# Optimization experiments

Hardware: AMD Instinct MI355X
Metric: run time of the kernel (lower is better)

Reference implementation:

```python
import jax, jax.numpy as jnp
import numpy as np

EPS = 1e-5      # F.layer_norm default eps
ALPHA = 0.08    # ALALLaDA blend coefficient


def setup_inputs() -> dict:
    key = jax.random.key(0)
    ks = jax.random.split(key, 6)
    B, S, D, K = 2, 2048, 2048, 8
    Fh = D // 4
    h_L = jax.random.normal(ks[0], (B, S, D), jnp.float32)
    # nonzero -> masked position (stands in for input_ids == 126336)
    mask = jax.random.randint(ks[1], (B, S), 0, 2).astype(jnp.int32)
    Wr = jax.random.normal(ks[2], (K, D), jnp.float32) / np.sqrt(D).astype(np.float32)
    br = jnp.zeros((K,), jnp.float32)
    W1 = jax.random.normal(ks[3], (K, D, Fh), jnp.float32) / np.sqrt(D).astype(np.float32)
    b1 = jnp.zeros((K, Fh), jnp.float32)
    W2 = jax.random.normal(ks[4], (K, Fh, D), jnp.float32) / np.sqrt(Fh).astype(np.float32)
    b2 = jnp.zeros((K, D), jnp.float32)
    return {"h_L": h_L, "mask": mask, "Wr": Wr, "br": br,
            "W1": W1, "b1": b1, "W2": W2, "b2": b2, "range_r": 8}


def _router_blend(h_L, Wr, br, W1, b1, W2, b2, mask, range_r):
    B, S, D = h_L.shape
    masked = mask != 0
    um = (~masked).astype(h_L.dtype)  # unmasked validity [B,S]
    # Per-token, per-expert outputs M[b,s,k,d]: Linear -> exact GELU -> Linear.
    pre = jnp.einsum('bsd,kdf->bskf', h_L, W1) + b1
    M = jnp.einsum('bskf,kfd->bskd', jax.nn.gelu(pre, approximate=False), W2) + b2
    # Routing weights at every position (softmax over K experts).
    w = jax.nn.softmax(jnp.einsum('bsd,kd->bsk', h_L, Wr) + br, axis=-1)
    # Accumulate weighted expert outputs over the +/-range_r neighbor window,
    # counting only unmasked neighbors. Fixed small loop over 2r offsets.
    num = jnp.zeros((B, S, D), h_L.dtype)
    cnt = jnp.zeros((B, S), h_L.dtype)
    for o in range(-range_r, range_r + 1):
        if o == 0:
            continue
        if o > 0:  # neighbor t = a + o: shift left, zero-pad tail
            Mo = jnp.pad(M[:, o:], ((0, 0), (0, o), (0, 0), (0, 0)))
            vo = jnp.pad(um[:, o:], ((0, 0), (0, o)))
        else:      # neighbor t = a + o (o<0): shift right, zero-pad head
            Mo = jnp.pad(M[:, :o], ((0, 0), (-o, 0), (0, 0), (0, 0)))
            vo = jnp.pad(um[:, :o], ((0, 0), (-o, 0)))
        num = num + vo[..., None] * jnp.einsum('bsk,bskd->bsd', w, Mo)
        cnt = cnt + vo
    has = cnt > 0
    mean = num / jnp.maximum(cnt, 1.0)[..., None]   # mean over valid neighbors
    # layer_norm over d_model, no affine
    mu = mean.mean(-1, keepdims=True)
    var = jnp.mean((mean - mu) ** 2, axis=-1, keepdims=True)
    ln = (mean - mu) / jnp.sqrt(var + EPS)
    # delta is written only at masked positions that had >=1 neighbor
    delta = jnp.where((masked & has)[..., None], ln, 0.0)
    return h_L + ALPHA * delta


def reference(h_L, mask, Wr, br, W1, b1, W2, b2, range_r):
    return _router_blend(h_L, Wr, br, W1, b1, W2, b2, mask, range_r)
```

## Files before the change

kernel.cpp:

```cpp
#include <hip/hip_runtime.h>
#include <hip/hip_bf16.h>
#include <math.h>


#define ALPHA 0.08f
#define EPS 1e-5f

typedef __attribute__((ext_vector_type(8))) __bf16 bf16x8;
typedef __attribute__((ext_vector_type(8))) short short8;
typedef __attribute__((ext_vector_type(4))) float f32x4;

__device__ __forceinline__ unsigned short f2bf(float f) {
  unsigned u = __float_as_uint(f);
  u += 0x7fffu + ((u >> 16) & 1u);
  return (unsigned short)(u >> 16);
}
__device__ __forceinline__ float bf2f(unsigned short b) {
  return __uint_as_float(((unsigned)b) << 16);
}

#define GLD16(gptr, lptr)                                                     \
  __builtin_amdgcn_global_load_lds(                                           \
      (const __attribute__((address_space(1))) void*)(gptr),                  \
      (__attribute__((address_space(3))) void*)(lptr), 16, 0, 0)

__device__ __forceinline__ int wave_incl_scan(int v, int lane) {
#pragma unroll
  for (int off = 1; off < 64; off <<= 1) {
    int t = __shfl_up(v, off);
    if (lane >= off) v += t;
  }
  return v;
}

__global__ __launch_bounds__(1024) void scan_kernel(
    const int* __restrict__ mask, const int* __restrict__ rptr,
    int* __restrict__ ru, int* __restrict__ unm_idx,
    int* __restrict__ msk_idx, int* __restrict__ pos2row,
    int* __restrict__ counts) {
  __shared__ int sru[4097];
  __shared__ int wsum[16];
  __shared__ int wsum2[17];
  const int tid = threadIdx.x;
  const int lane = tid & 63, wv = tid >> 6;
  const int t0 = tid * 4;
  const int4 m4 = *(const int4*)(mask + t0);
  int f[4];
  f[0] = (m4.x == 0); f[1] = (m4.y == 0); f[2] = (m4.z == 0); f[3] = (m4.w == 0);
  const int tsum = f[0] + f[1] + f[2] + f[3];
  const int isc = wave_incl_scan(tsum, lane);
  if (lane == 63) wsum[wv] = isc;
  __syncthreads();
  if (tid == 0) {
    int acc = 0;
#pragma unroll
    for (int i = 0; i < 16; ++i) { int v = wsum[i]; wsum[i] = acc; acc += v; }
    sru[4096] = acc;
    counts[0] = acc;
    ru[4096] = acc;
  }
  __syncthreads();
  int ex = wsum[wv] + isc - tsum;
#pragma unroll
  for (int j = 0; j < 4; ++j) {
    sru[t0 + j] = ex;
    ru[t0 + j] = ex;
    if (f[j]) unm_idx[ex] = t0 + j;
    ex += f[j];
  }
  __syncthreads();
  const int r = rptr[0];
  int mval[4] = {m4.x, m4.y, m4.z, m4.w};
  int g[4];
#pragma unroll
  for (int j = 0; j < 4; ++j) {
    const int t = t0 + j;
    const int s = t & 2047, tb = t & ~2047;
    const int lo = max(s - r, 0), hi = min(s + r, 2047);
    const int cnt = sru[tb + hi + 1] - sru[tb + lo];
    g[j] = (mval[j] != 0 && cnt > 0) ? 1 : 0;
  }
  const int tsum2 = g[0] + g[1] + g[2] + g[3];
  const int isc2 = wave_incl_scan(tsum2, lane);
  if (lane == 63) wsum2[wv] = isc2;
  __syncthreads();
  if (tid == 0) {
    int acc = 0;
#pragma unroll
    for (int i = 0; i < 16; ++i) { int v = wsum2[i]; wsum2[i] = acc; acc += v; }
    counts[1] = acc;
  }
  __syncthreads();
  int ex2 = wsum2[wv] + isc2 - tsum2;
#pragma unroll
  for (int j = 0; j < 4; ++j) {
    const int t = t0 + j;
    pos2row[t] = g[j] ? ex2 : -1;
    if (g[j]) msk_idx[ex2] = t;
    ex2 += g[j];
  }
}

__global__ void packrouter_kernel(const float* __restrict__ h,
                                  const int* __restrict__ mask,
                                  const int* __restrict__ ru,
                                  const float* __restrict__ Wr,
                                  const float* __restrict__ br,
                                  float* __restrict__ w,
                                  unsigned short* __restrict__ hbc) {
  const int a = blockIdx.x;
  const int tid = threadIdx.x;
  const int lane = tid & 63, wid = tid >> 6;
  const size_t base = (size_t)a * 2048;
  const int d0 = tid * 8;
  float hv[8];
  *(float4*)(hv) = *(const float4*)(h + base + d0);
  *(float4*)(hv + 4) = *(const float4*)(h + base + d0 + 4);
  float acc[8];
#pragma unroll
  for (int k = 0; k < 8; ++k) {
    float wvv[8];
    *(float4*)(wvv) = *(const float4*)(Wr + (size_t)k * 2048 + d0);
    *(float4*)(wvv + 4) = *(const float4*)(Wr + (size_t)k * 2048 + d0 + 4);
    float s = 0.f;
#pragma unroll
    for (int j = 0; j < 8; ++j) s += hv[j] * wvv[j];
    acc[k] = s;
  }
#pragma unroll
  for (int off = 32; off > 0; off >>= 1)
#pragma unroll
    for (int k = 0; k < 8; ++k) acc[k] += __shfl_down(acc[k], off);
  __shared__ float red[4][8];
  __shared__ float logits[8];
  if (lane == 0)
#pragma unroll
    for (int k = 0; k < 8; ++k) red[wid][k] = acc[k];
  __syncthreads();
  if (tid < 8)
    logits[tid] = red[0][tid] + red[1][tid] + red[2][tid] + red[3][tid] + br[tid];
  __syncthreads();
  if (tid == 0) {
    float mx = logits[0];
#pragma unroll
    for (int k = 1; k < 8; ++k) mx = fmaxf(mx, logits[k]);
    float e[8], se = 0.f;
#pragma unroll
    for (int k = 0; k < 8; ++k) {
      e[k] = expf(logits[k] - mx);
      se += e[k];
    }
    const float is = 1.f / se;
#pragma unroll
    for (int k = 0; k < 8; ++k) w[(size_t)a * 8 + k] = e[k] * is;
  }
  if (mask[a] == 0) {
    const int i = ru[a];
    short8 o;
#pragma unroll
    for (int j = 0; j < 8; ++j) o[j] = (short)f2bf(hv[j]);
    *(short8*)(hbc + (size_t)i * 2048 + d0) = o;
  }
}

__global__ void transpose_pack_kernel(const float* __restrict__ src,
                                      unsigned short* __restrict__ dst,
                                      int R, int C, size_t dstStride,
                                      size_t dstExpStride) {
  __shared__ float tile[32][33];
  const int k = blockIdx.z;
  src += (size_t)k * (size_t)R * (size_t)C;
  dst += (size_t)k * dstExpStride;
  const int c0 = blockIdx.x * 32;
  const int r0 = blockIdx.y * 32;
  const int tx = threadIdx.x;
  const int ty = threadIdx.y;
#pragma unroll
  for (int i = 0; i < 4; ++i)
    tile[ty + 8 * i][tx] = src[(size_t)(r0 + ty + 8 * i) * C + (c0 + tx)];
  __syncthreads();
#pragma unroll
  for (int i = 0; i < 4; ++i) {
    const int c = c0 + ty + 8 * i;
    dst[(size_t)c * dstStride + (size_t)(r0 + tx)] = f2bf(tile[tx][ty + 8 * i]);
  }
}

template <int EPI>
__global__ __launch_bounds__(256, 2) void gemm_bt_kernel(
    const unsigned short* __restrict__ A, const unsigned short* __restrict__ Bt,
    float* __restrict__ Cf, unsigned short* __restrict__ Cb,
    const float* __restrict__ bias, const int* __restrict__ counts, int cidx,
    int N, int Kd) {
  const int Mlim = counts[cidx];
  const int bm = blockIdx.y * 128;
  if (bm >= Mlim) return;
  __shared__ __align__(16) unsigned short L[4][8192];
  const int tid = threadIdx.x;
  const int lane = tid & 63;
  const int wid = tid >> 6;
  const int bn = blockIdx.x * 128;
  const int wr = wid >> 1;
  const int wc = wid & 1;

  f32x4 acc[4][4];
#pragma unroll
  for (int m = 0; m < 4; ++m)
#pragma unroll
    for (int n = 0; n < 4; ++n) acc[m][n] = (f32x4){0.f, 0.f, 0.f, 0.f};

  const int srow = wid * 16 + (lane >> 2);
  const int scol = (lane & 3) * 8;
  const unsigned short* gA0 = A + (size_t)(bm + srow) * Kd + scol;
  const unsigned short* gA1 = gA0 + (size_t)64 * Kd;
  const unsigned short* gB0 = Bt + (size_t)(bn + srow) * Kd + scol;
  const unsigned short* gB1 = gB0 + (size_t)64 * Kd;

  const int aoff = (wr * 64 + (lane & 15)) * 32 + (lane >> 4) * 8;
  const int boff = (wc * 64 + (lane & 15)) * 32 + (lane >> 4) * 8;

#define STAGE(buf, t)                                                         \
  {                                                                           \
    const int k0_ = (t) << 5;                                                 \
    unsigned short* la_ = &L[(buf)][0] + wid * 512;                           \
    unsigned short* lb_ = &L[(buf)][4096] + wid * 512;                        \
    GLD16(gA0 + k0_, la_);                                                    \
    GLD16(gA1 + k0_, la_ + 2048);                                             \
    GLD16(gB0 + k0_, lb_);                                                    \
    GLD16(gB1 + k0_, lb_ + 2048);                                             \
  }

#define COMPUTE(buf)                                                          \
  {                                                                           \
    const unsigned short* As_ = &L[(buf)][0];                                 \
    const unsigned short* Bs_ = &L[(buf)][4096];                              \
    bf16x8 af[4], bfr[4];                                                     \
    _Pragma("unroll") for (int m = 0; m < 4; ++m) af[m] =                     \
        __builtin_bit_cast(bf16x8, *(const short8*)(As_ + aoff + m * 512));   \
    _Pragma("unroll") for (int n = 0; n < 4; ++n) bfr[n] =                    \
        __builtin_bit_cast(bf16x8, *(const short8*)(Bs_ + boff + n * 512));   \
    _Pragma("unroll") for (int m = 0; m < 4; ++m)                             \
        _Pragma("unroll") for (int n = 0; n < 4; ++n) acc[m][n] =             \
            __builtin_amdgcn_mfma_f32_16x16x32_bf16(af[m], bfr[n],            \
                                                    acc[m][n], 0, 0, 0);      \
  }

  const int nt = Kd >> 5;
  STAGE(0, 0);
  STAGE(1, 1);
  STAGE(2, 2);
#pragma unroll 1
  for (int t = 0; t < nt - 3; ++t) {
    asm volatile("s_waitcnt vmcnt(8)" ::: "memory");
    __builtin_amdgcn_s_barrier();
    __builtin_amdgcn_sched_barrier(0);
    STAGE((t + 3) & 3, t + 3);
    COMPUTE(t & 3);
  }
  {
    asm volatile("s_waitcnt vmcnt(8)" ::: "memory");
    __builtin_amdgcn_s_barrier();
    __builtin_amdgcn_sched_barrier(0);
    COMPUTE((nt - 3) & 3);
  }
  {
    asm volatile("s_waitcnt vmcnt(4)" ::: "memory");
    __builtin_amdgcn_s_barrier();
    __builtin_amdgcn_sched_barrier(0);
    COMPUTE((nt - 2) & 3);
  }
  {
    asm volatile("s_waitcnt vmcnt(0)" ::: "memory");
    __builtin_amdgcn_s_barrier();
    __builtin_amdgcn_sched_barrier(0);
    COMPUTE((nt - 1) & 3);
  }
#undef STAGE
#undef COMPUTE

  const int r0 = bm + wr * 64 + (lane >> 4) * 4;
  const int c0 = bn + wc * 64 + (lane & 15);
#pragma unroll
  for (int m = 0; m < 4; ++m) {
#pragma unroll
    for (int n = 0; n < 4; ++n) {
      const int col = c0 + n * 16;
#pragma unroll
      for (int i = 0; i < 4; ++i) {
        const int row = r0 + m * 16 + i;
        if (row >= Mlim) continue;
        const size_t off = (size_t)row * N + col;
        float v = acc[m][n][i];
        if (EPI == 1) {
          v += bias[col];
          v = 0.5f * v * (1.0f + erff(v * 0.70710678118654752f));
          Cb[off] = f2bf(v);
        } else {
          Cf[off] = v;
        }
      }
    }
  }
}

__global__ void window_kernel(const unsigned short* __restrict__ Act_c,
                              const float* __restrict__ w,
                              const int* __restrict__ msk_idx,
                              const int* __restrict__ ru,
                              const int* __restrict__ rptr,
                              const int* __restrict__ counts,
                              unsigned short* __restrict__ G_c) {
  const int i = blockIdx.y;
  if (i >= counts[1]) return;
  const int a = msk_idx[i];
  const int s = a & 2047;
  const int tb = a & ~2047;
  const int r = rptr[0];
  const int lo = max(s - r, 0), hi = min(s + r, 2047);
  const int jlo = ru[tb + lo], jhi = ru[tb + hi + 1];
  const int c = blockIdx.x * 2048 + threadIdx.x * 8;
  float acc[8] = {0.f, 0.f, 0.f, 0.f, 0.f, 0.f, 0.f, 0.f};
  for (int j = jlo; j < jhi; ++j) {
    const short8 v = *(const short8*)(Act_c + (size_t)j * 4096 + c);
#pragma unroll
    for (int jj = 0; jj < 8; ++jj) acc[jj] += bf2f((unsigned short)v[jj]);
  }
  const float wv = w[(size_t)a * 8 + (c >> 9)];
  short8 o8;
#pragma unroll
  for (int jj = 0; jj < 8; ++jj) o8[jj] = (short)f2bf(acc[jj] * wv);
  *(short8*)(G_c + (size_t)i * 4096 + c) = o8;
}

__global__ void final_kernel(const float* __restrict__ h,
                             const int* __restrict__ pos2row,
                             const float* __restrict__ w,
                             const float* __restrict__ b2,
                             const float* __restrict__ num_c,
                             const int* __restrict__ ru,
                             const int* __restrict__ rptr,
                             float* __restrict__ out) {
  const int a = blockIdx.x;
  const int tid = threadIdx.x;
  const int lane = tid & 63, wid = tid >> 6;
  const size_t base = (size_t)a * 2048;
  const int d0 = tid * 8;
  const int row = pos2row[a];
  if (row < 0) {
    const float4 x0 = *(const float4*)(h + base + d0);
    const float4 x1 = *(const float4*)(h + base + d0 + 4);
    *(float4*)(out + base + d0) = x0;
    *(float4*)(out + base + d0 + 4) = x1;
    return;
  }
  const int s = a & 2047;
  const int tb = a & ~2047;
  const int r = rptr[0];
  const int lo = max(s - r, 0), hi = min(s + r, 2047);
  const int cnt = ru[tb + hi + 1] - ru[tb + lo];
  float wk[8];
#pragma unroll
  for (int k = 0; k < 8; ++k) wk[k] = w[(size_t)a * 8 + k];
  const float cntf = (float)cnt;
  const float icnt = 1.0f / cntf;
  float mval[8];
  float s1 = 0.f, s2 = 0.f;
#pragma unroll
  for (int j = 0; j < 8; ++j) {
    const int d = d0 + j;
    float wb2 = 0.f;
#pragma unroll
    for (int k = 0; k < 8; ++k) wb2 += wk[k] * b2[(size_t)k * 2048 + d];
    const float v = (num_c[(size_t)row * 2048 + d] + cntf * wb2) * icnt;
    mval[j] = v;
    s1 += v;
    s2 += v * v;
  }
#pragma unroll
  for (int off = 32; off > 0; off >>= 1) {
    s1 += __shfl_down(s1, off);
    s2 += __shfl_down(s2, off);
  }
  __shared__ float red[8];
  if (lane == 0) {
    red[wid] = s1;
    red[4 + wid] = s2;
  }
  __syncthreads();
  const float S1 = red[0] + red[1] + red[2] + red[3];
  const float S2 = red[4] + red[5] + red[6] + red[7];
  const float mu = S1 * (1.0f / 2048.0f);
  const float var = S2 * (1.0f / 2048.0f) - mu * mu;
  const float rin = rsqrtf(var + EPS);
#pragma unroll
  for (int j = 0; j < 8; ++j) {
    const int d = d0 + j;
    out[base + d] = h[base + d] + ALPHA * ((mval[j] - mu) * rin);
  }
}

extern "C" void kernel_launch(void* const* d_in, const int* in_sizes, int n_in,
                              void* d_out, int out_size, void* d_ws,
                              size_t ws_size, hipStream_t stream) {
  const float* h = (const float*)d_in[0];
  const int* mask = (const int*)d_in[1];
  const float* Wr = (const float*)d_in[2];
  const float* br = (const float*)d_in[3];
  const float* W1 = (const float*)d_in[4];
  const float* b1 = (const float*)d_in[5];
  const float* W2 = (const float*)d_in[6];
  const float* b2 = (const float*)d_in[7];
  const int* rptr = (const int*)d_in[8];
  float* out = (float*)d_out;

  char* ws = (char*)d_ws;
  unsigned short* hbc = (unsigned short*)(ws + 0);
  unsigned short* B1t = (unsigned short*)(ws + 16777216);
  unsigned short* B2t = (unsigned short*)(ws + 33554432);
  unsigned short* Act_c = (unsigned short*)(ws + 50331648);
  unsigned short* G_c = (unsigned short*)(ws + 83886080);
  float* num_c = (float*)(ws + 50331648);
  float* wbuf = (float*)(ws + 117440512);
  int* ru = (int*)(ws + 117571584);
  int* unm_idx = ru + 4100;
  int* msk_idx = unm_idx + 4096;
  int* pos2row = msk_idx + 4096;
  int* counts = pos2row + 4096;

  scan_kernel<<<1, 1024, 0, stream>>>(mask, rptr, ru, unm_idx, msk_idx,
                                      pos2row, counts);
  packrouter_kernel<<<4096, 256, 0, stream>>>(h, mask, ru, Wr, br, wbuf, hbc);
  transpose_pack_kernel<<<dim3(16, 64, 8), dim3(32, 8), 0, stream>>>(
      W1, B1t, 2048, 512, 2048, (size_t)512 * 2048);
  transpose_pack_kernel<<<dim3(64, 16, 8), dim3(32, 8), 0, stream>>>(
      W2, B2t, 512, 2048, 4096, 512);
  gemm_bt_kernel<1><<<dim3(32, 32), 256, 0, stream>>>(
      hbc, B1t, nullptr, Act_c, b1, counts, 0, 4096, 2048);
  window_kernel<<<dim3(2, 4096), 256, 0, stream>>>(Act_c, wbuf, msk_idx, ru,
                                                   rptr, counts, G_c);
  gemm_bt_kernel<0><<<dim3(16, 32), 256, 0, stream>>>(
      G_c, B2t, num_c, nullptr, nullptr, counts, 1, 2048, 4096);
  final_kernel<<<4096, 256, 0, stream>>>(h, pos2row, wbuf, b2, num_c, ru,
                                         rptr, out);
}
```

Before: 346.7 us.

## Fuse prep kernels, widen GEMM K-tile with swizzled LDS, interleave window rows

Merges the scan, router/pack and two weight-transpose kernels into one launch. Each router block now computes its own compaction index by counting unmasked positions before it, which removes the dependency on a separate scan. The GEMM moves from a 4-stage K=32 pipeline to a 2-stage K=64 pipeline with an XOR-swizzled LDS layout to cut bank conflicts and barriers per K. The window kernel remaps block indices to interleave rows across blocks. The trade-offs are redundant mask reads in every router block and less load-latency hiding in the shallower GEMM pipeline.

```diff
diff --git a/kernel.cpp b/kernel.cpp
--- a/kernel.cpp
+++ b/kernel.cpp
@@ -33,156 +33,199 @@
   return v;
 }
 
-__global__ __launch_bounds__(1024) void scan_kernel(
-    const int* __restrict__ mask, const int* __restrict__ rptr,
-    int* __restrict__ ru, int* __restrict__ unm_idx,
+__global__ __launch_bounds__(256) void prep_kernel(
+    const float* __restrict__ h, const int* __restrict__ mask,
+    const float* __restrict__ Wr, const float* __restrict__ br,
+    const float* __restrict__ W1, const float* __restrict__ W2,
+    const int* __restrict__ rptr, float* __restrict__ w,
+    unsigned short* __restrict__ hbc, unsigned short* __restrict__ B1t,
+    unsigned short* __restrict__ B2t, int* __restrict__ ru,
     int* __restrict__ msk_idx, int* __restrict__ pos2row,
     int* __restrict__ counts) {
-  __shared__ int sru[4097];
-  __shared__ int wsum[16];
-  __shared__ int wsum2[17];
+  const int bid = blockIdx.x;
   const int tid = threadIdx.x;
   const int lane = tid & 63, wv = tid >> 6;
-  const int t0 = tid * 4;
-  const int4 m4 = *(const int4*)(mask + t0);
-  int f[4];
-  f[0] = (m4.x == 0); f[1] = (m4.y == 0); f[2] = (m4.z == 0); f[3] = (m4.w == 0);
-  const int tsum = f[0] + f[1] + f[2] + f[3];
-  const int isc = wave_incl_scan(tsum, lane);
-  if (lane == 63) wsum[wv] = isc;
-  __syncthreads();
-  if (tid == 0) {
-    int acc = 0;
-#pragma unroll
-    for (int i = 0; i < 16; ++i) { int v = wsum[i]; wsum[i] = acc; acc += v; }
-    sru[4096] = acc;
-    counts[0] = acc;
-    ru[4096] = acc;
-  }
-  __syncthreads();
-  int ex = wsum[wv] + isc - tsum;
-#pragma unroll
-  for (int j = 0; j < 4; ++j) {
-    sru[t0 + j] = ex;
-    ru[t0 + j] = ex;
-    if (f[j]) unm_idx[ex] = t0 + j;
-    ex += f[j];
-  }
-  __syncthreads();
-  const int r = rptr[0];
-  int mval[4] = {m4.x, m4.y, m4.z, m4.w};
-  int g[4];
-#pragma unroll
-  for (int j = 0; j < 4; ++j) {
-    const int t = t0 + j;
-    const int s = t & 2047, tb = t & ~2047;
-    const int lo = max(s - r, 0), hi = min(s + r, 2047);
-    const int cnt = sru[tb + hi + 1] - sru[tb + lo];
-    g[j] = (mval[j] != 0 && cnt > 0) ? 1 : 0;
-  }
-  const int tsum2 = g[0] + g[1] + g[2] + g[3];
-  const int isc2 = wave_incl_scan(tsum2, lane);
-  if (lane == 63) wsum2[wv] = isc2;
-  __syncthreads();
-  if (tid == 0) {
-    int acc = 0;
-#pragma unroll
-    for (int i = 0; i < 16; ++i) { int v = wsum2[i]; wsum2[i] = acc; acc += v; }
-    counts[1] = acc;
-  }
-  __syncthreads();
-  int ex2 = wsum2[wv] + isc2 - tsum2;
-#pragma unroll
-  for (int j = 0; j < 4; ++j) {
-    const int t = t0 + j;
-    pos2row[t] = g[j] ? ex2 : -1;
-    if (g[j]) msk_idx[ex2] = t;
-    ex2 += g[j];
-  }
-}
-
-__global__ void packrouter_kernel(const float* __restrict__ h,
-                                  const int* __restrict__ mask,
-                                  const int* __restrict__ ru,
-                                  const float* __restrict__ Wr,
-                                  const float* __restrict__ br,
-                                  float* __restrict__ w,
-                                  unsigned short* __restrict__ hbc) {
-  const int a = blockIdx.x;
-  const int tid = threadIdx.x;
-  const int lane = tid & 63, wid = tid >> 6;
-  const size_t base = (size_t)a * 2048;
-  const int d0 = tid * 8;
-  float hv[8];
-  *(float4*)(hv) = *(const float4*)(h + base + d0);
-  *(float4*)(hv + 4) = *(const float4*)(h + base + d0 + 4);
-  float acc[8];
-#pragma unroll
-  for (int k = 0; k < 8; ++k) {
-    float wvv[8];
-    *(float4*)(wvv) = *(const float4*)(Wr + (size_t)k * 2048 + d0);
-    *(float4*)(wvv + 4) = *(const float4*)(Wr + (size_t)k * 2048 + d0 + 4);
-    float s = 0.f;
-#pragma unroll
-    for (int j = 0; j < 8; ++j) s += hv[j] * wvv[j];
-    acc[k] = s;
-  }
-#pragma unroll
-  for (int off = 32; off > 0; off >>= 1)
-#pragma unroll
-    for (int k = 0; k < 8; ++k) acc[k] += __shfl_down(acc[k], off);
-  __shared__ float red[4][8];
-  __shared__ float logits[8];
-  if (lane == 0)
-#pragma unroll
-    for (int k = 0; k < 8; ++k) red[wid][k] = acc[k];
-  __syncthreads();
-  if (tid < 8)
-    logits[tid] = red[0][tid] + red[1][tid] + red[2][tid] + red[3][tid] + br[tid];
-  __syncthreads();
-  if (tid == 0) {
-    float mx = logits[0];
-#pragma unroll
-    for (int k = 1; k < 8; ++k) mx = fmaxf(mx, logits[k]);
-    float e[8], se = 0.f;
+
+  if (bid < 16384) {
+    __shared__ float tile[32][33];
+    int id = bid;
+    const float* src;
+    unsigned short* dst;
+    int C, c0, r0;
+    size_t dstStride;
+    if (id < 8192) {
+      const int k = id >> 10, rem = id & 1023;
+      src = W1 + (size_t)k * 2048 * 512;
+      dst = B1t + (size_t)k * 512 * 2048;
+      C = 512; dstStride = 2048;
+      c0 = (rem >> 6) * 32; r0 = (rem & 63) * 32;
+    } else {
+      id -= 8192;
+      const int k = id >> 10, rem = id & 1023;
+      src = W2 + (size_t)k * 512 * 2048;
+      dst = B2t + (size_t)k * 512;
+      C = 2048; dstStride = 4096;
+      c0 = (rem >> 4) * 32; r0 = (rem & 15) * 32;
+    }
+    const int tx = tid & 31, ty = tid >> 5;
+#pragma unroll
+    for (int i = 0; i < 4; ++i)
+      tile[ty + 8 * i][tx] = src[(size_t)(r0 + ty + 8 * i) * C + (c0 + tx)];
+    __syncthreads();
+#pragma unroll
+    for (int i = 0; i < 4; ++i) {
+      const int c = c0 + ty + 8 * i;
+      dst[(size_t)c * dstStride + (size_t)(r0 + tx)] =
+          f2bf(tile[tx][ty + 8 * i]);
+    }
+    return;
+  }
+
+  if (bid < 20480) {
+    const int a = bid - 16384;
+    const size_t base = (size_t)a * 2048;
+    const int d0 = tid * 8;
+    float hv[8];
+    *(float4*)(hv) = *(const float4*)(h + base + d0);
+    *(float4*)(hv + 4) = *(const float4*)(h + base + d0 + 4);
+    float acc[8];
 #pragma unroll
     for (int k = 0; k < 8; ++k) {
-      e[k] = expf(logits[k] - mx);
-      se += e[k];
-    }
-    const float is = 1.f / se;
-#pragma unroll
-    for (int k = 0; k < 8; ++k) w[(size_t)a * 8 + k] = e[k] * is;
-  }
-  if (mask[a] == 0) {
-    const int i = ru[a];
-    short8 o;
-#pragma unroll
-    for (int j = 0; j < 8; ++j) o[j] = (short)f2bf(hv[j]);
-    *(short8*)(hbc + (size_t)i * 2048 + d0) = o;
-  }
-}
-
-__global__ void transpose_pack_kernel(const float* __restrict__ src,
-                                      unsigned short* __restrict__ dst,
-                                      int R, int C, size_t dstStride,
-                                      size_t dstExpStride) {
-  __shared__ float tile[32][33];
-  const int k = blockIdx.z;
-  src += (size_t)k * (size_t)R * (size_t)C;
-  dst += (size_t)k * dstExpStride;
-  const int c0 = blockIdx.x * 32;
-  const int r0 = blockIdx.y * 32;
-  const int tx = threadIdx.x;
-  const int ty = threadIdx.y;
-#pragma unroll
-  for (int i = 0; i < 4; ++i)
-    tile[ty + 8 * i][tx] = src[(size_t)(r0 + ty + 8 * i) * C + (c0 + tx)];
-  __syncthreads();
-#pragma unroll
-  for (int i = 0; i < 4; ++i) {
-    const int c = c0 + ty + 8 * i;
-    dst[(size_t)c * dstStride + (size_t)(r0 + tx)] = f2bf(tile[tx][ty + 8 * i]);
+      float wvv[8];
+      *(float4*)(wvv) = *(const float4*)(Wr + (size_t)k * 2048 + d0);
+      *(float4*)(wvv + 4) = *(const float4*)(Wr + (size_t)k * 2048 + d0 + 4);
+      float s = 0.f;
+#pragma unroll
+      for (int j = 0; j < 8; ++j) s += hv[j] * wvv[j];
+      acc[k] = s;
+    }
+    int c0n = 0;
+    {
+      const int4* m4p = (const int4*)mask;
+#pragma unroll
+      for (int q = 0; q < 4; ++q) {
+        const int4 v = m4p[tid * 4 + q];
+        const int b0 = tid * 16 + q * 4;
+        c0n += (v.x == 0 && b0 + 0 < a);
+        c0n += (v.y == 0 && b0 + 1 < a);
+        c0n += (v.z == 0 && b0 + 2 < a);
+        c0n += (v.w == 0 && b0 + 3 < a);
+      }
+    }
+#pragma unroll
+    for (int off = 32; off > 0; off >>= 1) {
+      c0n += __shfl_down(c0n, off);
+#pragma unroll
+      for (int k = 0; k < 8; ++k) acc[k] += __shfl_down(acc[k], off);
+    }
+    __shared__ float red[4][8];
+    __shared__ float logits[8];
+    __shared__ int rucnt[4];
+    __shared__ int rubc;
+    if (lane == 0) {
+#pragma unroll
+      for (int k = 0; k < 8; ++k) red[wv][k] = acc[k];
+      rucnt[wv] = c0n;
+    }
+    __syncthreads();
+    if (tid < 8)
+      logits[tid] =
+          red[0][tid] + red[1][tid] + red[2][tid] + red[3][tid] + br[tid];
+    if (tid == 0) rubc = rucnt[0] + rucnt[1] + rucnt[2] + rucnt[3];
+    __syncthreads();
+    if (tid == 0) {
+      float mx = logits[0];
+#pragma unroll
+      for (int k = 1; k < 8; ++k) mx = fmaxf(mx, logits[k]);
+      float e[8], se = 0.f;
+#pragma unroll
+      for (int k = 0; k < 8; ++k) {
+        e[k] = expf(logits[k] - mx);
+        se += e[k];
+      }
+      const float is = 1.f / se;
+#pragma unroll
+      for (int k = 0; k < 8; ++k) w[(size_t)a * 8 + k] = e[k] * is;
+    }
+    if (mask[a] == 0) {
+      const int i = rubc;
+      short8 o;
+#pragma unroll
+      for (int j = 0; j < 8; ++j) o[j] = (short)f2bf(hv[j]);
+      *(short8*)(hbc + (size_t)i * 2048 + d0) = o;
+    }
+    return;
+  }
+
+  {
+    __shared__ int sru[4097];
+    __shared__ int wsum[4];
+    __shared__ int wsum2[4];
+    const int t0 = tid * 16;
+    int mv[16];
+    {
+      const int4* p = (const int4*)mask;
+#pragma unroll
+      for (int q = 0; q < 4; ++q) {
+        const int4 v = p[tid * 4 + q];
+        mv[q * 4 + 0] = v.x; mv[q * 4 + 1] = v.y;
+        mv[q * 4 + 2] = v.z; mv[q * 4 + 3] = v.w;
+      }
+    }
+    int f[16];
+    int c = 0;
+#pragma unroll
+    for (int e = 0; e < 16; ++e) { f[e] = (mv[e] == 0); c += f[e]; }
+    const int isc = wave_incl_scan(c, lane);
+    if (lane == 63) wsum[wv] = isc;
+    __syncthreads();
+    if (tid == 0) {
+      int accs = 0;
+#pragma unroll
+      for (int i = 0; i < 4; ++i) { int v = wsum[i]; wsum[i] = accs; accs += v; }
+      sru[4096] = accs;
+      ru[4096] = accs;
+      counts[0] = accs;
+    }
+    __syncthreads();
+    int ex = wsum[wv] + isc - c;
+#pragma unroll
+    for (int e = 0; e < 16; ++e) {
+      sru[t0 + e] = ex;
+      ru[t0 + e] = ex;
+      ex += f[e];
+    }
+    __syncthreads();
+    const int r = rptr[0];
+    int g[16];
+    int c2 = 0;
+#pragma unroll
+    for (int e = 0; e < 16; ++e) {
+      const int t = t0 + e;
+      const int s = t & 2047, tb = t & ~2047;
+      const int lo = max(s - r, 0), hi = min(s + r, 2047);
+      const int cnt = sru[tb + hi + 1] - sru[tb + lo];
+      g[e] = (mv[e] != 0 && cnt > 0) ? 1 : 0;
+      c2 += g[e];
+    }
+    const int isc2 = wave_incl_scan(c2, lane);
+    if (lane == 63) wsum2[wv] = isc2;
+    __syncthreads();
+    if (tid == 0) {
+      int accs = 0;
+#pragma unroll
+      for (int i = 0; i < 4; ++i) { int v = wsum2[i]; wsum2[i] = accs; accs += v; }
+      counts[1] = accs;
+    }
+    __syncthreads();
+    int ex2 = wsum2[wv] + isc2 - c2;
+#pragma unroll
+    for (int e = 0; e < 16; ++e) {
+      const int t = t0 + e;
+      pos2row[t] = g[e] ? ex2 : -1;
+      if (g[e]) msk_idx[ex2] = t;
+      ex2 += g[e];
+    }
   }
 }
 
@@ -195,7 +238,7 @@
   const int Mlim = counts[cidx];
   const int bm = blockIdx.y * 128;
   if (bm >= Mlim) return;
-  __shared__ __align__(16) unsigned short L[4][8192];
+  __shared__ __align__(16) unsigned short L[2][16384];
   const int tid = threadIdx.x;
   const int lane = tid & 63;
   const int wid = tid >> 6;
@@ -209,72 +252,79 @@
 #pragma unroll
     for (int n = 0; n < 4; ++n) acc[m][n] = (f32x4){0.f, 0.f, 0.f, 0.f};
 
-  const int srow = wid * 16 + (lane >> 2);
-  const int scol = (lane & 3) * 8;
-  const unsigned short* gA0 = A + (size_t)(bm + srow) * Kd + scol;
-  const unsigned short* gA1 = gA0 + (size_t)64 * Kd;
-  const unsigned short* gB0 = Bt + (size_t)(bn + srow) * Kd + scol;
-  const unsigned short* gB1 = gB0 + (size_t)64 * Kd;
-
-  const int aoff = (wr * 64 + (lane & 15)) * 32 + (lane >> 4) * 8;
-  const int boff = (wc * 64 + (lane & 15)) * 32 + (lane >> 4) * 8;
+  const int l8 = lane >> 3;
+  const int scol = ((lane & 7) ^ l8) * 8;
+  const unsigned short* gA = A + (size_t)(bm + wid * 32 + l8) * Kd + scol;
+  const unsigned short* gB = Bt + (size_t)(bn + wid * 32 + l8) * Kd + scol;
+
+  const int arow = (wr * 64 + (lane & 15)) * 64;
+  const int brow = (wc * 64 + (lane & 15)) * 64;
+  const int t16 = lane >> 4;
+  const int x7 = lane & 7;
+  const int s0 = (t16 ^ x7) * 8;
+  const int s1 = ((4 + t16) ^ x7) * 8;
 
 #define STAGE(buf, t)                                                         \
   {                                                                           \
-    const int k0_ = (t) << 5;                                                 \
-    unsigned short* la_ = &L[(buf)][0] + wid * 512;                           \
-    unsigned short* lb_ = &L[(buf)][4096] + wid * 512;                        \
-    GLD16(gA0 + k0_, la_);                                                    \
-    GLD16(gA1 + k0_, la_ + 2048);                                             \
-    GLD16(gB0 + k0_, lb_);                                                    \
-    GLD16(gB1 + k0_, lb_ + 2048);                                             \
+    const int k0_ = (t) << 6;                                                 \
+    unsigned short* la_ = &L[(buf)][0] + wid * 2048;                          \
+    unsigned short* lb_ = &L[(buf)][8192] + wid * 2048;                       \
+    GLD16(gA + k0_, la_);                                                     \
+    GLD16(gA + (size_t)8 * Kd + k0_, la_ + 512);                              \
+    GLD16(gA + (size_t)16 * Kd + k0_, la_ + 1024);                            \
+    GLD16(gA + (size_t)24 * Kd + k0_, la_ + 1536);                            \
+    GLD16(gB + k0_, lb_);                                                     \
+    GLD16(gB + (size_t)8 * Kd + k0_, lb_ + 512);                              \
+    GLD16(gB + (size_t)16 * Kd + k0_, lb_ + 1024);                            \
+    GLD16(gB + (size_t)24 * Kd + k0_, lb_ + 1536);                            \
   }
 
 #define COMPUTE(buf)                                                          \
   {                                                                           \
     const unsigned short* As_ = &L[(buf)][0];                                 \
-    const unsigned short* Bs_ = &L[(buf)][4096];                              \
-    bf16x8 af[4], bfr[4];                                                     \
-    _Pragma("unroll") for (int m = 0; m < 4; ++m) af[m] =                     \
-        __builtin_bit_cast(bf16x8, *(const short8*)(As_ + aoff + m * 512));   \
-    _Pragma("unroll") for (int n = 0; n < 4; ++n) bfr[n] =                    \
-        __builtin_bit_cast(bf16x8, *(const short8*)(Bs_ + boff + n * 512));   \
+    const unsigned short* Bs_ = &L[(buf)][8192];                              \
+    bf16x8 a0[4], a1[4], b0[4], b1[4];                                        \
+    _Pragma("unroll") for (int m = 0; m < 4; ++m) {                           \
+      a0[m] = __builtin_bit_cast(bf16x8,                                      \
+                                 *(const short8*)(As_ + arow + m * 1024 + s0)); \
+      a1[m] = __builtin_bit_cast(bf16x8,                                      \
+                                 *(const short8*)(As_ + arow + m * 1024 + s1)); \
+    }                                                                         \
+    _Pragma("unroll") for (int n = 0; n < 4; ++n) {                           \
+      b0[n] = __builtin_bit_cast(bf16x8,                                      \
+                                 *(const short8*)(Bs_ + brow + n * 1024 + s0)); \
+      b1[n] = __builtin_bit_cast(bf16x8,                                      \
+                                 *(const short8*)(Bs_ + brow + n * 1024 + s1)); \
+    }                                                                         \
     _Pragma("unroll") for (int m = 0; m < 4; ++m)                             \
-        _Pragma("unroll") for (int n = 0; n < 4; ++n) acc[m][n] =             \
-            __builtin_amdgcn_mfma_f32_16x16x32_bf16(af[m], bfr[n],            \
-                                                    acc[m][n], 0, 0, 0);      \
-  }
-
-  const int nt = Kd >> 5;
+        _Pragma("unroll") for (int n = 0; n < 4; ++n) {                       \
+      acc[m][n] = __builtin_amdgcn_mfma_f32_16x16x32_bf16(a0[m], b0[n],       \
+                                                          acc[m][n], 0, 0, 0); \
+      acc[m][n] = __builtin_amdgcn_mfma_f32_16x16x32_bf16(a1[m], b1[n],       \
+                                                          acc[m][n], 0, 0, 0); \
+    }                                                                         \
+  }
+
+  const int nt = Kd >> 6;
   STAGE(0, 0);
   STAGE(1, 1);
-  STAGE(2, 2);
 #pragma unroll 1
-  for (int t = 0; t < nt - 3; ++t) {
+  for (int t = 0; t < nt - 2; ++t) {
     asm volatile("s_waitcnt vmcnt(8)" ::: "memory");
     __builtin_amdgcn_s_barrier();
     __builtin_amdgcn_sched_barrier(0);
-    STAGE((t + 3) & 3, t + 3);
-    COMPUTE(t & 3);
-  }
-  {
-    asm volatile("s_waitcnt vmcnt(8)" ::: "memory");
+    COMPUTE(t & 1);
     __builtin_amdgcn_s_barrier();
-    __builtin_amdgcn_sched_barrier(0);
-    COMPUTE((nt - 3) & 3);
-  }
-  {
-    asm volatile("s_waitcnt vmcnt(4)" ::: "memory");
-    __builtin_amdgcn_s_barrier();
-    __builtin_amdgcn_sched_barrier(0);
-    COMPUTE((nt - 2) & 3);
-  }
-  {
-    asm volatile("s_waitcnt vmcnt(0)" ::: "memory");
-    __builtin_amdgcn_s_barrier();
-    __builtin_amdgcn_sched_barrier(0);
-    COMPUTE((nt - 1) & 3);
-  }
+    STAGE(t & 1, t + 2);
+  }
+  asm volatile("s_waitcnt vmcnt(8)" ::: "memory");
+  __builtin_amdgcn_s_barrier();
+  __builtin_amdgcn_sched_barrier(0);
+  COMPUTE(nt & 1);
+  asm volatile("s_waitcnt vmcnt(0)" ::: "memory");
+  __builtin_amdgcn_s_barrier();
+  __builtin_amdgcn_sched_barrier(0);
+  COMPUTE((nt - 1) & 1);
 #undef STAGE
 #undef COMPUTE
 
@@ -310,8 +360,13 @@
                               const int* __restrict__ rptr,
                               const int* __restrict__ counts,
                               unsigned short* __restrict__ G_c) {
-  const int i = blockIdx.y;
-  if (i >= counts[1]) return;
+  const int Nm = counts[1];
+  const int o = blockIdx.y;
+  const int q = (Nm + 7) >> 3;
+  const int y = o >> 3;
+  if (y >= q) return;
+  const int i = (o & 7) * q + y;
+  if (i >= Nm) return;
   const int a = msk_idx[i];
   const int s = a & 2047;
   const int tb = a & ~2047;
@@ -422,18 +477,13 @@
   float* num_c = (float*)(ws + 50331648);
   float* wbuf = (float*)(ws + 117440512);
   int* ru = (int*)(ws + 117571584);
-  int* unm_idx = ru + 4100;
-  int* msk_idx = unm_idx + 4096;
+  int* msk_idx = ru + 4100;
   int* pos2row = msk_idx + 4096;
   int* counts = pos2row + 4096;
 
-  scan_kernel<<<1, 1024, 0, stream>>>(mask, rptr, ru, unm_idx, msk_idx,
-                                      pos2row, counts);
-  packrouter_kernel<<<4096, 256, 0, stream>>>(h, mask, ru, Wr, br, wbuf, hbc);
-  transpose_pack_kernel<<<dim3(16, 64, 8), dim3(32, 8), 0, stream>>>(
-      W1, B1t, 2048, 512, 2048, (size_t)512 * 2048);
-  transpose_pack_kernel<<<dim3(64, 16, 8), dim3(32, 8), 0, stream>>>(
-      W2, B2t, 512, 2048, 4096, 512);
+  prep_kernel<<<20481, 256, 0, stream>>>(h, mask, Wr, br, W1, W2, rptr, wbuf,
+                                         hbc, B1t, B2t, ru, msk_idx, pos2row,
+                                         counts);
   gemm_bt_kernel<1><<<dim3(32, 32), 256, 0, stream>>>(
       hbc, B1t, nullptr, Act_c, b1, counts, 0, 4096, 2048);
   window_kernel<<<dim3(2, 4096), 256, 0, stream>>>(Act_c, wbuf, msk_idx, ru,
```

After: 308.5 us. 1.12x faster.
